# Kernel optimization log

Measured on AMD Instinct MI355X. Metric: run time of the kernel, lower is better.

Reference implementation:

```python
import jax, jax.numpy as jnp
import numpy as np

B, Z, C, H, W = 512, 256, 3, 64, 64
DATASET_SIZE = 737280
LOG2PI = float(np.log(2.0 * np.pi))


def setup_inputs() -> dict:
    key = jax.random.key(0)
    k1, k2, k3, k4, k5 = jax.random.split(key, 5)
    # pixel data / reconstructions in (0,1) for bernoulli BCE (avoid log(0))
    data = jax.random.uniform(k1, (B, C, H, W), dtype=jnp.float32) * 0.98 + 0.01
    recon_batch = jax.random.uniform(k2, (B, C, H, W), dtype=jnp.float32) * 0.98 + 0.01
    latent_sample = jax.random.normal(k3, (B, Z), dtype=jnp.float32)
    mu = jax.random.normal(k4, (B, Z), dtype=jnp.float32) * 0.1
    logvar = jax.random.normal(k5, (B, Z), dtype=jnp.float32) * 0.1
    return {"data": data, "recon_batch": recon_batch, "latent_sample": latent_sample,
            "mu": mu, "logvar": logvar, "dataset_size": DATASET_SIZE}


def _log_density_normal(sample, mu, logvar):
    # NOTE: faithful to source: inv_var = exp(logvar) (repo quirk, not exp(-logvar))
    return -0.5 * ((sample - mu) ** 2 * jnp.exp(logvar) + logvar + LOG2PI)


def reference(data, recon_batch, latent_sample, mu, logvar, dataset_size):
    bsz = data.shape[0]
    # bernoulli reconstruction loss (BCE summed, normalized per batch)
    rec_loss = -jnp.sum(data * jnp.log(recon_batch)
                        + (1.0 - data) * jnp.log(1.0 - recon_batch)) / bsz
    # dimension-wise KL (faithful to source: exp(logvar + mu^2))
    dw_kl_loss = jnp.mean(jnp.sum(-0.5 * logvar
                                  + 0.5 * jnp.exp(logvar + mu ** 2) - 0.5, axis=1))
    # pairwise log q(z_i | x_j): [B, B, Z]
    logqz_mat = _log_density_normal(latent_sample[:, None, :],
                                    mu[None, :, :], logvar[None, :, :])
    log_norm = float(np.log(bsz)) + jnp.log(jnp.asarray(dataset_size, jnp.float32))
    # sum_k [ logsumexp_j logq(i,j,k) - log(B*N) ]
    logqz_prodmarginals = jnp.sum(jax.nn.logsumexp(logqz_mat, axis=1) - log_norm, axis=1)
    # logsumexp_j sum_k logq(i,j,k) - log(B*N)
    logqz = jax.nn.logsumexp(jnp.sum(logqz_mat, axis=2), axis=1) - log_norm
    tc_loss = jnp.mean(logqz - logqz_prodmarginals)
    elbo = rec_loss + tc_loss + dw_kl_loss
    return elbo
```

## Files before the change

kernel.cpp:

```cpp
#include <hip/hip_runtime.h>

#define BATCH 512
#define ZDIM 256


__device__ __forceinline__ float fast_exp2(float x) {
#if __has_builtin(__builtin_amdgcn_exp2f)
    return __builtin_amdgcn_exp2f(x);
#else
    return exp2f(x);
#endif
}

__device__ __forceinline__ float wave_reduce_sum(float v) {
#pragma unroll
    for (int off = 32; off > 0; off >>= 1)
        v += __shfl_down(v, off, 64);
    return v;
}

__device__ __forceinline__ float wave_reduce_max(float v) {
#pragma unroll
    for (int off = 32; off > 0; off >>= 1)
        v = fmaxf(v, __shfl_down(v, off, 64));
    return v;
}

__device__ __forceinline__ float block_sum256(float v, float* red) {
    float w = wave_reduce_sum(v);
    if ((threadIdx.x & 63) == 0) red[threadIdx.x >> 6] = w;
    __syncthreads();
    float r = red[0] + red[1] + red[2] + red[3];
    __syncthreads();
    return r;
}


__global__ __launch_bounds__(256) void k_tables(
    const float* __restrict__ mu, const float* __restrict__ logvar,
    float2* __restrict__ evl, float2* __restrict__ e2wT,
    float* __restrict__ cj, float* __restrict__ dwrow,
    unsigned int* __restrict__ cnt) {
    __shared__ float red[4];
    int j = blockIdx.x, k = threadIdx.x;
    if (j == 0 && k == 0) cnt[0] = 0u;
    float m = mu[j * ZDIM + k];
    float lv = logvar[j * ZDIM + k];
    float ev = __expf(lv);
    float e2n = -0.5f * ev;
    float lcn = -0.5f * (lv + 1.8378770664093453f);
    const float L2E = 1.4426950408889634f;
    evl[j * ZDIM + k] = make_float2(e2n * L2E, lcn * L2E);
    e2wT[k * BATCH + j] = make_float2(e2n, m * ev);
    float cpart = m * m * e2n + lcn;
    float csum = block_sum256(cpart, red);
    if (k == 0) cj[j] = csum;
    float dw = -0.5f * lv + 0.5f * __expf(lv + m * m) - 0.5f;
    float dsum = block_sum256(dw, red);
    if (k == 0) dwrow[j] = dsum;
}

__global__ __launch_bounds__(256) void k_bulk(
    const float4* __restrict__ d, const float4* __restrict__ r,
    const float* __restrict__ lat, const float2* __restrict__ evl,
    const float* __restrict__ mu, float* __restrict__ part,
    const float2* __restrict__ e2wT, const float* __restrict__ cj,
    float* __restrict__ smat, float* __restrict__ recpart) {
    __shared__ float ss[4 * ZDIM];
    int b = blockIdx.x, t = threadIdx.x;
    if (b < 512) {
        __shared__ float red[4];
        float s = 0.f;
        int base = b * 256 + t;
#pragma unroll 4
        for (int it = 0; it < 12; ++it) {
            int idx = base + it * 131072;
            float4 dv = d[idx];
            float4 rv = r[idx];
            s += dv.x * __logf(rv.x) + (1.f - dv.x) * __logf(1.f - rv.x);
            s += dv.y * __logf(rv.y) + (1.f - dv.y) * __logf(1.f - rv.y);
            s += dv.z * __logf(rv.z) + (1.f - dv.z) * __logf(1.f - rv.z);
            s += dv.w * __logf(rv.w) + (1.f - dv.w) * __logf(1.f - rv.w);
        }
        float tot = block_sum256(s, red);
        if (t == 0) recpart[b] = tot;
    } else if (b < 1024) {
        int pb = b - 512;
        int i0 = (pb >> 3) * 8, j0 = (pb & 7) * 64;
        float s[8], a[8];
#pragma unroll
        for (int i = 0; i < 8; i++) {
            s[i] = lat[(i0 + i) * ZDIM + t];
            a[i] = 0.f;
        }
        for (int j = j0; j < j0 + 64; j++) {
            float2 el = evl[j * ZDIM + t];
            float m = mu[j * ZDIM + t];
#pragma unroll
            for (int i = 0; i < 8; i++) {
                float dd = s[i] - m;
                float v = fmaf(dd * dd, el.x, el.y);
                a[i] += fast_exp2(v);
            }
        }
#pragma unroll
        for (int i = 0; i < 8; i++)
            part[((pb & 7) * BATCH + i0 + i) * ZDIM + t] = a[i];
    } else {
        int sb = b - 1024;
        int i0 = (sb >> 1) * 4;
        int j = (sb & 1) * 256 + t;
        for (int idx = t; idx < 4 * ZDIM; idx += 256)
            ss[idx] = lat[i0 * ZDIM + idx];
        __syncthreads();
        float a0 = 0.f, a1 = 0.f, a2 = 0.f, a3 = 0.f;
#pragma unroll 4
        for (int k = 0; k < ZDIM; k++) {
            float2 ew = e2wT[k * BATCH + j];
            float s0 = ss[0 * ZDIM + k];
            float s1 = ss[1 * ZDIM + k];
            float s2 = ss[2 * ZDIM + k];
            float s3 = ss[3 * ZDIM + k];
            a0 = fmaf(s0, fmaf(s0, ew.x, ew.y), a0);
            a1 = fmaf(s1, fmaf(s1, ew.x, ew.y), a1);
            a2 = fmaf(s2, fmaf(s2, ew.x, ew.y), a2);
            a3 = fmaf(s3, fmaf(s3, ew.x, ew.y), a3);
        }
        float c = cj[j];
        smat[(i0 + 0) * BATCH + j] = a0 + c;
        smat[(i0 + 1) * BATCH + j] = a1 + c;
        smat[(i0 + 2) * BATCH + j] = a2 + c;
        smat[(i0 + 3) * BATCH + j] = a3 + c;
    }
}

__global__ __launch_bounds__(256) void k_finalize(
    const float* __restrict__ part, const float* __restrict__ smat,
    const int* __restrict__ dsz, const float* __restrict__ recpart,
    const float* __restrict__ dwrow, float* __restrict__ tcpart,
    unsigned int* __restrict__ cnt, float* __restrict__ out) {
    __shared__ float red[4];
    int i = blockIdx.x, t = threadIdx.x;
    float s = 0.f;
#pragma unroll
    for (int jc = 0; jc < 8; jc++)
        s += part[(jc * BATCH + i) * ZDIM + t];
    float prod_i = block_sum256(__logf(s), red);
    float v1 = smat[i * BATCH + t];
    float v2 = smat[i * BATCH + 256 + t];
    float m = wave_reduce_max(fmaxf(v1, v2));
    if ((t & 63) == 0) red[t >> 6] = m;
    __syncthreads();
    m = fmaxf(fmaxf(red[0], red[1]), fmaxf(red[2], red[3]));
    __syncthreads();
    float e = __expf(v1 - m) + __expf(v2 - m);
    float sum = block_sum256(e, red);
    __shared__ bool amLast;
    if (t == 0) {
        float log_norm = __logf(512.f) + __logf((float)dsz[0]);
        float logqz = m + __logf(sum) - log_norm;
        float pm = prod_i - 256.f * log_norm;
        __hip_atomic_store(&tcpart[i], logqz - pm, __ATOMIC_RELAXED,
                           __HIP_MEMORY_SCOPE_AGENT);
        unsigned int old = __hip_atomic_fetch_add(cnt, 1u, __ATOMIC_ACQ_REL,
                                                  __HIP_MEMORY_SCOPE_AGENT);
        amLast = (old == BATCH - 1);
    }
    __syncthreads();
    if (amLast) {
        float acc = 0.f;
        float tc1 = __hip_atomic_load(&tcpart[t], __ATOMIC_RELAXED,
                                      __HIP_MEMORY_SCOPE_AGENT);
        float tc2 = __hip_atomic_load(&tcpart[t + 256], __ATOMIC_RELAXED,
                                      __HIP_MEMORY_SCOPE_AGENT);
        acc += tc1 + tc2;
        acc += dwrow[t] + dwrow[t + 256];
        acc -= recpart[t] + recpart[t + 256];
        float tot = block_sum256(acc, red);
        if (t == 0) out[0] = tot * (1.f / 512.f);
    }
}


extern "C" void kernel_launch(void* const* d_in, const int* in_sizes, int n_in,
                              void* d_out, int out_size, void* d_ws, size_t ws_size,
                              hipStream_t stream) {
    const float* data   = (const float*)d_in[0];
    const float* recon  = (const float*)d_in[1];
    const float* lat    = (const float*)d_in[2];
    const float* mu     = (const float*)d_in[3];
    const float* logvar = (const float*)d_in[4];
    const int*   dsz    = (const int*)d_in[5];
    float* out = (float*)d_out;

    float*  ws      = (float*)d_ws;
    unsigned int* cnt = (unsigned int*)ws;
    float*  recpart = ws + 64;
    float*  dwrow   = recpart + 512;
    float*  tcpart  = dwrow + 512;
    float*  cj      = tcpart + 512;
    float2* evl     = (float2*)(ws + 4096);
    float2* e2wT    = (float2*)(ws + 4096 + 262144);
    float*  part    = ws + 4096 + 524288;
    float*  smat    = part + 1048576;

    k_tables<<<512, 256, 0, stream>>>(mu, logvar, evl, e2wT, cj, dwrow, cnt);
    k_bulk<<<1280, 256, 0, stream>>>((const float4*)data, (const float4*)recon,
                                     lat, evl, mu, part, e2wT, cj, smat, recpart);
    k_finalize<<<512, 256, 0, stream>>>(part, smat, dsz, recpart, dwrow,
                                        tcpart, cnt, out);
}
```

Baseline: 132.4 us.

## Expand pairwise quadratic into precomputed coefficients and widen smat tiles to 16 rows

The per-dimension pairwise term is expanded as a*s^2 + b*s + c, with a, b and c precomputed per (j,k) into a float4 table. The exp loop then does one 16-byte load instead of two loads and a subtract-square. The smat blocks now compute 16 latent rows each from a transposed shared tile, read as float4, instead of 4 rows. This raises reuse of the e2wT loads and cuts the block count from 256 to 64. The trade-offs are a larger shared-memory footprint (16 KB per block), more registers, fewer blocks in the smat phase, and a possible precision loss from expanding the square.

Result: slower. 154.6 us (+16.8%).

```diff
diff --git a/kernel.cpp b/kernel.cpp
--- a/kernel.cpp
+++ b/kernel.cpp
@@ -38,7 +38,7 @@
 
 __global__ __launch_bounds__(256) void k_tables(
     const float* __restrict__ mu, const float* __restrict__ logvar,
-    float2* __restrict__ evl, float2* __restrict__ e2wT,
+    float4* __restrict__ abc, float2* __restrict__ e2wT,
     float* __restrict__ cj, float* __restrict__ dwrow,
     unsigned int* __restrict__ cnt) {
     __shared__ float red[4];
@@ -50,9 +50,9 @@
     float e2n = -0.5f * ev;
     float lcn = -0.5f * (lv + 1.8378770664093453f);
     const float L2E = 1.4426950408889634f;
-    evl[j * ZDIM + k] = make_float2(e2n * L2E, lcn * L2E);
+    float cpart = m * m * e2n + lcn;
+    abc[j * ZDIM + k] = make_float4(e2n * L2E, m * ev * L2E, cpart * L2E, 0.f);
     e2wT[k * BATCH + j] = make_float2(e2n, m * ev);
-    float cpart = m * m * e2n + lcn;
     float csum = block_sum256(cpart, red);
     if (k == 0) cj[j] = csum;
     float dw = -0.5f * lv + 0.5f * __expf(lv + m * m) - 0.5f;
@@ -62,14 +62,13 @@
 
 __global__ __launch_bounds__(256) void k_bulk(
     const float4* __restrict__ d, const float4* __restrict__ r,
-    const float* __restrict__ lat, const float2* __restrict__ evl,
-    const float* __restrict__ mu, float* __restrict__ part,
+    const float* __restrict__ lat, const float4* __restrict__ abc,
+    float* __restrict__ part,
     const float2* __restrict__ e2wT, const float* __restrict__ cj,
     float* __restrict__ smat, float* __restrict__ recpart) {
-    __shared__ float ss[4 * ZDIM];
+    __shared__ float ss[16 * ZDIM];
     int b = blockIdx.x, t = threadIdx.x;
     if (b < 512) {
-        __shared__ float red[4];
         float s = 0.f;
         int base = b * 256 + t;
 #pragma unroll 4
@@ -82,24 +81,23 @@
             s += dv.z * __logf(rv.z) + (1.f - dv.z) * __logf(1.f - rv.z);
             s += dv.w * __logf(rv.w) + (1.f - dv.w) * __logf(1.f - rv.w);
         }
-        float tot = block_sum256(s, red);
+        float tot = block_sum256(s, ss);
         if (t == 0) recpart[b] = tot;
     } else if (b < 1024) {
         int pb = b - 512;
         int i0 = (pb >> 3) * 8, j0 = (pb & 7) * 64;
-        float s[8], a[8];
+        float s[8], s2[8], a[8];
 #pragma unroll
         for (int i = 0; i < 8; i++) {
             s[i] = lat[(i0 + i) * ZDIM + t];
+            s2[i] = s[i] * s[i];
             a[i] = 0.f;
         }
         for (int j = j0; j < j0 + 64; j++) {
-            float2 el = evl[j * ZDIM + t];
-            float m = mu[j * ZDIM + t];
+            float4 q = abc[j * ZDIM + t];
 #pragma unroll
             for (int i = 0; i < 8; i++) {
-                float dd = s[i] - m;
-                float v = fmaf(dd * dd, el.x, el.y);
+                float v = fmaf(s2[i], q.x, fmaf(s[i], q.y, q.z));
                 a[i] += fast_exp2(v);
             }
         }
@@ -108,29 +106,42 @@
             part[((pb & 7) * BATCH + i0 + i) * ZDIM + t] = a[i];
     } else {
         int sb = b - 1024;
-        int i0 = (sb >> 1) * 4;
+        int i0 = (sb >> 1) * 16;
         int j = (sb & 1) * 256 + t;
-        for (int idx = t; idx < 4 * ZDIM; idx += 256)
-            ss[idx] = lat[i0 * ZDIM + idx];
+        for (int n = 0; n < 16; n++) {
+            int idx = n * 256 + t;
+            ss[t * 16 + n] = lat[i0 * ZDIM + idx];
+        }
         __syncthreads();
-        float a0 = 0.f, a1 = 0.f, a2 = 0.f, a3 = 0.f;
-#pragma unroll 4
+        float acc[16];
+#pragma unroll
+        for (int i = 0; i < 16; i++) acc[i] = 0.f;
+#pragma unroll 2
         for (int k = 0; k < ZDIM; k++) {
             float2 ew = e2wT[k * BATCH + j];
-            float s0 = ss[0 * ZDIM + k];
-            float s1 = ss[1 * ZDIM + k];
-            float s2 = ss[2 * ZDIM + k];
-            float s3 = ss[3 * ZDIM + k];
-            a0 = fmaf(s0, fmaf(s0, ew.x, ew.y), a0);
-            a1 = fmaf(s1, fmaf(s1, ew.x, ew.y), a1);
-            a2 = fmaf(s2, fmaf(s2, ew.x, ew.y), a2);
-            a3 = fmaf(s3, fmaf(s3, ew.x, ew.y), a3);
+            const float4* sp = (const float4*)(ss + k * 16);
+            float4 s0 = sp[0], s1 = sp[1], s2v = sp[2], s3 = sp[3];
+            acc[0]  = fmaf(s0.x,  fmaf(s0.x,  ew.x, ew.y), acc[0]);
+            acc[1]  = fmaf(s0.y,  fmaf(s0.y,  ew.x, ew.y), acc[1]);
+            acc[2]  = fmaf(s0.z,  fmaf(s0.z,  ew.x, ew.y), acc[2]);
+            acc[3]  = fmaf(s0.w,  fmaf(s0.w,  ew.x, ew.y), acc[3]);
+            acc[4]  = fmaf(s1.x,  fmaf(s1.x,  ew.x, ew.y), acc[4]);
+            acc[5]  = fmaf(s1.y,  fmaf(s1.y,  ew.x, ew.y), acc[5]);
+            acc[6]  = fmaf(s1.z,  fmaf(s1.z,  ew.x, ew.y), acc[6]);
+            acc[7]  = fmaf(s1.w,  fmaf(s1.w,  ew.x, ew.y), acc[7]);
+            acc[8]  = fmaf(s2v.x, fmaf(s2v.x, ew.x, ew.y), acc[8]);
+            acc[9]  = fmaf(s2v.y, fmaf(s2v.y, ew.x, ew.y), acc[9]);
+            acc[10] = fmaf(s2v.z, fmaf(s2v.z, ew.x, ew.y), acc[10]);
+            acc[11] = fmaf(s2v.w, fmaf(s2v.w, ew.x, ew.y), acc[11]);
+            acc[12] = fmaf(s3.x,  fmaf(s3.x,  ew.x, ew.y), acc[12]);
+            acc[13] = fmaf(s3.y,  fmaf(s3.y,  ew.x, ew.y), acc[13]);
+            acc[14] = fmaf(s3.z,  fmaf(s3.z,  ew.x, ew.y), acc[14]);
+            acc[15] = fmaf(s3.w,  fmaf(s3.w,  ew.x, ew.y), acc[15]);
         }
         float c = cj[j];
-        smat[(i0 + 0) * BATCH + j] = a0 + c;
-        smat[(i0 + 1) * BATCH + j] = a1 + c;
-        smat[(i0 + 2) * BATCH + j] = a2 + c;
-        smat[(i0 + 3) * BATCH + j] = a3 + c;
+#pragma unroll
+        for (int i = 0; i < 16; i++)
+            smat[(i0 + i) * BATCH + j] = acc[i] + c;
     }
 }
 
@@ -199,14 +210,14 @@
     float*  dwrow   = recpart + 512;
     float*  tcpart  = dwrow + 512;
     float*  cj      = tcpart + 512;
-    float2* evl     = (float2*)(ws + 4096);
-    float2* e2wT    = (float2*)(ws + 4096 + 262144);
-    float*  part    = ws + 4096 + 524288;
+    float4* abc     = (float4*)(ws + 4096);
+    float2* e2wT    = (float2*)(ws + 4096 + 524288);
+    float*  part    = ws + 4096 + 786432;
     float*  smat    = part + 1048576;
 
-    k_tables<<<512, 256, 0, stream>>>(mu, logvar, evl, e2wT, cj, dwrow, cnt);
-    k_bulk<<<1280, 256, 0, stream>>>((const float4*)data, (const float4*)recon,
-                                     lat, evl, mu, part, e2wT, cj, smat, recpart);
+    k_tables<<<512, 256, 0, stream>>>(mu, logvar, abc, e2wT, cj, dwrow, cnt);
+    k_bulk<<<1088, 256, 0, stream>>>((const float4*)data, (const float4*)recon,
+                                     lat, abc, part, e2wT, cj, smat, recpart);
     k_finalize<<<512, 256, 0, stream>>>(part, smat, dsz, recpart, dwrow,
                                         tcpart, cnt, out);
 }
```
